# Kernel tuning notes

Hardware: AMD Instinct MI355X
Metric: run time of the kernel (lower is better)

Reference implementation:

```python
import jax, jax.numpy as jnp
from jax import lax
import numpy as np

NOTES = 78
IN_DIM = 80
T_HID = 64
N_HID = 2
B = 64
T = 128


def lstm_seq(x, w_ih, w_hh, b_ih, b_hh):
    """Batch-first single-layer LSTM from zero state.
    x: (N, S, D); w_ih: (4H, D); w_hh: (4H, H). Gate order i,f,g,o (PyTorch).
    Returns hidden outputs (N, S, H)."""
    H = w_hh.shape[1]
    N = x.shape[0]
    # precompute input contribution for all steps: (N, S, 4H)
    gx = jnp.einsum('nsd,gd->nsg', x, w_ih) + b_ih + b_hh

    def step(carry, g_t):
        h, c = carry
        g = g_t + h @ w_hh.T
        i, f, gg, o = jnp.split(g, 4, axis=-1)
        c = jax.nn.sigmoid(f) * c + jax.nn.sigmoid(i) * jnp.tanh(gg)
        h = jax.nn.sigmoid(o) * jnp.tanh(c)
        return (h, c), h

    h0 = jnp.zeros((N, H), x.dtype)
    (_, _), hs = lax.scan(step, (h0, h0), jnp.swapaxes(gx, 0, 1))
    return jnp.swapaxes(hs, 0, 1)  # (N, S, H)


def setup_inputs() -> dict:
    key = jax.random.key(0)
    ks = jax.random.split(key, 9)
    s = 1.0 / np.sqrt(T_HID)
    sn = 1.0 / np.sqrt(N_HID)
    u = lambda k, shp, sc: jax.random.uniform(k, shp, jnp.float32, -sc, sc)
    return {
        'x': jax.random.normal(ks[0], (B, NOTES, T, IN_DIM), jnp.float32),
        'w_ih_t': u(ks[1], (4 * T_HID, IN_DIM), s),
        'w_hh_t': u(ks[2], (4 * T_HID, T_HID), s),
        'b_ih_t': u(ks[3], (4 * T_HID,), s),
        'b_hh_t': u(ks[4], (4 * T_HID,), s),
        'w_ih_n': u(ks[5], (4 * N_HID, T_HID), sn),
        'w_hh_n': u(ks[6], (4 * N_HID, N_HID), sn),
        'b_ih_n': u(ks[7], (4 * N_HID,), sn),
        'b_hh_n': u(ks[8], (4 * N_HID,), sn),
    }


def reference(x, w_ih_t, w_hh_t, b_ih_t, b_hh_t, w_ih_n, w_hh_n, b_ih_n, b_hh_n):
    b, n_notes, t_len, _ = x.shape
    # Time LSTM: independent over (batch, note); sequence axis = time.
    xt = x.reshape(b * n_notes, t_len, IN_DIM)
    time_out = lstm_seq(xt, w_ih_t, w_hh_t, b_ih_t, b_hh_t)  # (B*78, T, H)
    time_out = time_out.reshape(b, n_notes, t_len, T_HID)
    # Note LSTM: run over the 78-note axis, fresh zero state at EVERY time step
    # (faithful to the original, which reuses self.hidden_note0 each iteration).
    xn = jnp.transpose(time_out, (0, 2, 1, 3)).reshape(b * t_len, n_notes, T_HID)
    note_out = lstm_seq(xn, w_ih_n, w_hh_n, b_ih_n, b_hh_n)  # (B*T, 78, 2)
    note_out = note_out.reshape(b, t_len, n_notes * N_HID)  # (B, T, 156)
    # Hard threshold, exactly as torch.where(x > 0.5, ones, zeros)
    return jnp.where(note_out > 0.5, jnp.ones_like(note_out), jnp.zeros_like(note_out))
```

## Files before the change

### kernel.cpp

```cpp
#include <hip/hip_runtime.h>
#include <math.h>

#define NOTES 78
#define IN_DIM 80
#define T_HID 64
#define N_HID 2
#define BATCH 64
#define TLEN 128
#define NSEQ (BATCH * NOTES)
#define NBT  (BATCH * TLEN)
#define SB   4

__device__ __forceinline__ float sigf(float x) { return 1.0f / (1.0f + expf(-x)); }
__device__ __forceinline__ float rdl(float v, int k) {
    return __int_as_float(__builtin_amdgcn_readlane(__float_as_int(v), k));
}

__global__ __launch_bounds__(256, 2)
void time_lstm_fused(const float* __restrict__ x,
                     const float* __restrict__ w_ih,
                     const float* __restrict__ w_hh,
                     const float* __restrict__ b_ih,
                     const float* __restrict__ b_hh,
                     const float* __restrict__ w_ih_n,
                     const float* __restrict__ b_ih_n,
                     const float* __restrict__ b_hh_n,
                     float* __restrict__ gxn) {
    __shared__ float hbuf[SB][T_HID];
    __shared__ float G0[SB][256];
    __shared__ float G1[SB][256];

    const int tid  = threadIdx.x;
    const int s0   = blockIdx.x * SB;
    const int wid  = tid >> 6;
    const int lane = tid & 63;
    const bool isx = (wid < 2);
    const int g0   = ((wid & 1) << 7) | (2 * lane);

    float4 wA[20], wB[20];
    float biasA = 0.0f, biasB = 0.0f;
    if (isx) {
        const float4* pA = (const float4*)(w_ih + (size_t)g0 * IN_DIM);
        const float4* pB = (const float4*)(w_ih + (size_t)(g0 + 1) * IN_DIM);
#pragma unroll
        for (int j = 0; j < 20; j++) { wA[j] = pA[j]; wB[j] = pB[j]; }
        biasA = b_ih[g0] + b_hh[g0];
        biasB = b_ih[g0 + 1] + b_hh[g0 + 1];
    } else {
        const float4* pA = (const float4*)(w_hh + (size_t)g0 * T_HID);
        const float4* pB = (const float4*)(w_hh + (size_t)(g0 + 1) * T_HID);
#pragma unroll
        for (int j = 0; j < 16; j++) { wA[j] = pA[j]; wB[j] = pB[j]; }
    }

    const float* xr[SB];
#pragma unroll
    for (int s = 0; s < SB; s++) xr[s] = x + (size_t)(s0 + s) * TLEN * IN_DIM;

    float xa[SB], xb[SB];
    if (isx) {
#pragma unroll
        for (int s = 0; s < SB; s++) {
            xa[s] = xr[s][lane];
            xb[s] = xr[s][64 + (lane & 15)];
        }
    }

    float cst = 0.0f;

    const int su2 = tid >> 6;
    const int nj  = (tid >> 3) & 7;
    const int nk  = tid & 7;
    float wn[8];
#pragma unroll
    for (int i = 0; i < 8; i++) wn[i] = w_ih_n[nj * 64 + nk * 8 + i];
    const float nbias = b_ih_n[nj] + b_hh_n[nj];
    const int sglb = s0 + su2;
    const int nb = sglb / NOTES, nn = sglb % NOTES;
    float* gout = gxn + ((size_t)nn * NBT + (size_t)nb * TLEN) * 8 + nj;

    hbuf[wid][lane] = 0.0f;
    __syncthreads();

    for (int t = 0; t < TLEN; t++) {
        if (t > 0) {
            float p = 0.0f;
#pragma unroll
            for (int i = 0; i < 8; i++) p = fmaf(wn[i], hbuf[su2][nk * 8 + i], p);
            p += __shfl_xor(p, 1);
            p += __shfl_xor(p, 2);
            p += __shfl_xor(p, 4);
            if (nk == 0) gout[(size_t)(t - 1) * 8] = p + nbias;
        }

        float xna[SB], xnb[SB];
        const bool pf = isx && (t + 1 < TLEN);
        if (pf) {
#pragma unroll
            for (int s = 0; s < SB; s++) {
                xna[s] = xr[s][(t + 1) * IN_DIM + lane];
                xnb[s] = xr[s][(t + 1) * IN_DIM + 64 + (lane & 15)];
            }
        }

        if (isx) {
            float aA[SB], aB[SB];
#pragma unroll
            for (int s = 0; s < SB; s++) { aA[s] = biasA; aB[s] = biasB; }
#pragma unroll
            for (int k4 = 0; k4 < 16; k4++) {
                const float4 vA = wA[k4], vB = wB[k4];
#pragma unroll
                for (int s = 0; s < SB; s++) {
                    const float r0 = rdl(xa[s], 4 * k4 + 0);
                    const float r1 = rdl(xa[s], 4 * k4 + 1);
                    const float r2 = rdl(xa[s], 4 * k4 + 2);
                    const float r3 = rdl(xa[s], 4 * k4 + 3);
                    aA[s] = fmaf(vA.x, r0, aA[s]);  aB[s] = fmaf(vB.x, r0, aB[s]);
                    aA[s] = fmaf(vA.y, r1, aA[s]);  aB[s] = fmaf(vB.y, r1, aB[s]);
                    aA[s] = fmaf(vA.z, r2, aA[s]);  aB[s] = fmaf(vB.z, r2, aB[s]);
                    aA[s] = fmaf(vA.w, r3, aA[s]);  aB[s] = fmaf(vB.w, r3, aB[s]);
                }
            }
#pragma unroll
            for (int k4 = 16; k4 < 20; k4++) {
                const float4 vA = wA[k4], vB = wB[k4];
#pragma unroll
                for (int s = 0; s < SB; s++) {
                    const float r0 = rdl(xb[s], 4 * k4 - 64);
                    const float r1 = rdl(xb[s], 4 * k4 - 63);
                    const float r2 = rdl(xb[s], 4 * k4 - 62);
                    const float r3 = rdl(xb[s], 4 * k4 - 61);
                    aA[s] = fmaf(vA.x, r0, aA[s]);  aB[s] = fmaf(vB.x, r0, aB[s]);
                    aA[s] = fmaf(vA.y, r1, aA[s]);  aB[s] = fmaf(vB.y, r1, aB[s]);
                    aA[s] = fmaf(vA.z, r2, aA[s]);  aB[s] = fmaf(vB.z, r2, aB[s]);
                    aA[s] = fmaf(vA.w, r3, aA[s]);  aB[s] = fmaf(vB.w, r3, aB[s]);
                }
            }
#pragma unroll
            for (int s = 0; s < SB; s++) {
                *(float2*)&G0[s][g0] = make_float2(aA[s], aB[s]);
            }
        } else {
            float hv[SB];
#pragma unroll
            for (int s = 0; s < SB; s++) hv[s] = hbuf[s][lane];
            float aA[SB], aB[SB];
#pragma unroll
            for (int s = 0; s < SB; s++) { aA[s] = 0.0f; aB[s] = 0.0f; }
#pragma unroll
            for (int k4 = 0; k4 < 16; k4++) {
                const float4 vA = wA[k4], vB = wB[k4];
#pragma unroll
                for (int s = 0; s < SB; s++) {
                    const float r0 = rdl(hv[s], 4 * k4 + 0);
                    const float r1 = rdl(hv[s], 4 * k4 + 1);
                    const float r2 = rdl(hv[s], 4 * k4 + 2);
                    const float r3 = rdl(hv[s], 4 * k4 + 3);
                    aA[s] = fmaf(vA.x, r0, aA[s]);  aB[s] = fmaf(vB.x, r0, aB[s]);
                    aA[s] = fmaf(vA.y, r1, aA[s]);  aB[s] = fmaf(vB.y, r1, aB[s]);
                    aA[s] = fmaf(vA.z, r2, aA[s]);  aB[s] = fmaf(vB.z, r2, aB[s]);
                    aA[s] = fmaf(vA.w, r3, aA[s]);  aB[s] = fmaf(vB.w, r3, aB[s]);
                }
            }
#pragma unroll
            for (int s = 0; s < SB; s++) {
                *(float2*)&G1[s][g0] = make_float2(aA[s], aB[s]);
            }
        }
        __syncthreads();

        {
            const float i_p = G0[wid][lane]       + G1[wid][lane];
            const float f_p = G0[wid][64 + lane]  + G1[wid][64 + lane];
            const float g_p = G0[wid][128 + lane] + G1[wid][128 + lane];
            const float o_p = G0[wid][192 + lane] + G1[wid][192 + lane];
            cst = sigf(f_p) * cst + sigf(i_p) * tanhf(g_p);
            const float h = sigf(o_p) * tanhf(cst);
            hbuf[wid][lane] = h;
        }
        if (pf) {
#pragma unroll
            for (int s = 0; s < SB; s++) { xa[s] = xna[s]; xb[s] = xnb[s]; }
        }
        __syncthreads();
    }

    {
        float p = 0.0f;
#pragma unroll
        for (int i = 0; i < 8; i++) p = fmaf(wn[i], hbuf[su2][nk * 8 + i], p);
        p += __shfl_xor(p, 1);
        p += __shfl_xor(p, 2);
        p += __shfl_xor(p, 4);
        if (nk == 0) gout[(size_t)(TLEN - 1) * 8] = p + nbias;
    }
}

__global__ __launch_bounds__(64)
void note_scan_kernel(const float* __restrict__ gxn,
                      const float* __restrict__ w_hh_n,
                      float* __restrict__ out) {
    const int bt = blockIdx.x * 64 + threadIdx.x;
    float wh[16];
#pragma unroll
    for (int i = 0; i < 16; i++) wh[i] = w_hh_n[i];
    float h0 = 0.f, h1 = 0.f, c0 = 0.f, c1 = 0.f;

    const float4* gp = (const float4*)gxn;
    float res[2 * NOTES];

    size_t idx = (size_t)bt * 2;
    float4 ga = gp[idx], gb = gp[idx + 1];
    for (int n = 0; n < NOTES; n++) {
        float4 na, nb2;
        if (n + 1 < NOTES) {
            const size_t nidx = ((size_t)(n + 1) * NBT + bt) * 2;
            na  = gp[nidx];
            nb2 = gp[nidx + 1];
        }
        const float i0 = ga.x + wh[0]  * h0 + wh[1]  * h1;
        const float i1 = ga.y + wh[2]  * h0 + wh[3]  * h1;
        const float f0 = ga.z + wh[4]  * h0 + wh[5]  * h1;
        const float f1 = ga.w + wh[6]  * h0 + wh[7]  * h1;
        const float g0 = gb.x + wh[8]  * h0 + wh[9]  * h1;
        const float g1 = gb.y + wh[10] * h0 + wh[11] * h1;
        const float o0 = gb.z + wh[12] * h0 + wh[13] * h1;
        const float o1 = gb.w + wh[14] * h0 + wh[15] * h1;
        c0 = sigf(f0) * c0 + sigf(i0) * tanhf(g0);
        c1 = sigf(f1) * c1 + sigf(i1) * tanhf(g1);
        h0 = sigf(o0) * tanhf(c0);
        h1 = sigf(o1) * tanhf(c1);
        res[n * 2 + 0] = (h0 > 0.5f) ? 1.0f : 0.0f;
        res[n * 2 + 1] = (h1 > 0.5f) ? 1.0f : 0.0f;
        ga = na; gb = nb2;
    }
    float4* op = (float4*)(out + (size_t)bt * (NOTES * N_HID));
#pragma unroll
    for (int j = 0; j < (2 * NOTES) / 4; j++) {
        op[j] = make_float4(res[4 * j], res[4 * j + 1], res[4 * j + 2], res[4 * j + 3]);
    }
}

extern "C" void kernel_launch(void* const* d_in, const int* in_sizes, int n_in,
                              void* d_out, int out_size, void* d_ws, size_t ws_size,
                              hipStream_t stream) {
    const float* x      = (const float*)d_in[0];
    const float* w_ih_t = (const float*)d_in[1];
    const float* w_hh_t = (const float*)d_in[2];
    const float* b_ih_t = (const float*)d_in[3];
    const float* b_hh_t = (const float*)d_in[4];
    const float* w_ih_n = (const float*)d_in[5];
    const float* w_hh_n = (const float*)d_in[6];
    const float* b_ih_n = (const float*)d_in[7];
    const float* b_hh_n = (const float*)d_in[8];
    float* out = (float*)d_out;

    float* gxn = (float*)d_ws;

    time_lstm_fused<<<NSEQ / SB, 256, 0, stream>>>(
        x, w_ih_t, w_hh_t, b_ih_t, b_hh_t, w_ih_n, b_ih_n, b_hh_n, gxn);
    note_scan_kernel<<<NBT / 64, 64, 0, stream>>>(gxn, w_hh_n, out);
}
```

Measured before the change: 1.354 ms.

## Split LSTM gate dot products across K-halves with 512-thread blocks

Doubles the time-LSTM block to 8 waves, so each wave handles half of the reduction dimension for the input and recurrent matvecs. Partial sums go to separate shared buffers and are added by the recurrent waves before the gate nonlinearity. This halves per-wave weight registers and serial FMA/readlane chains per step, which shortens the sequential critical path and may raise occupancy. The cost is extra shared-memory traffic and larger blocks. The note-scan kernel is also changed to write results incrementally as float4 instead of buffering 156 values in a register array.

```diff
diff --git a/kernel.cpp b/kernel.cpp
--- a/kernel.cpp
+++ b/kernel.cpp
@@ -16,7 +16,7 @@
     return __int_as_float(__builtin_amdgcn_readlane(__float_as_int(v), k));
 }
 
-__global__ __launch_bounds__(256, 2)
+__global__ __launch_bounds__(512, 4)
 void time_lstm_fused(const float* __restrict__ x,
                      const float* __restrict__ w_ih,
                      const float* __restrict__ w_hh,
@@ -27,88 +27,79 @@
                      const float* __restrict__ b_hh_n,
                      float* __restrict__ gxn) {
     __shared__ float hbuf[SB][T_HID];
-    __shared__ float G0[SB][256];
-    __shared__ float G1[SB][256];
+    __shared__ float Gx[2][SB][256];
+    __shared__ float Gh[2][SB][256];
 
     const int tid  = threadIdx.x;
     const int s0   = blockIdx.x * SB;
     const int wid  = tid >> 6;
     const int lane = tid & 63;
-    const bool isx = (wid < 2);
-    const int g0   = ((wid & 1) << 7) | (2 * lane);
-
-    float4 wA[20], wB[20];
+    const bool isx = (wid < 4);
+    const int lw   = isx ? wid : (wid - 4);
+    const int kh   = lw >> 1;
+    const int gh   = lw & 1;
+    const int g0   = (gh << 7) | (2 * lane);
+
+    float4 wA[10], wB[10];
     float biasA = 0.0f, biasB = 0.0f;
     if (isx) {
-        const float4* pA = (const float4*)(w_ih + (size_t)g0 * IN_DIM);
-        const float4* pB = (const float4*)(w_ih + (size_t)(g0 + 1) * IN_DIM);
-#pragma unroll
-        for (int j = 0; j < 20; j++) { wA[j] = pA[j]; wB[j] = pB[j]; }
-        biasA = b_ih[g0] + b_hh[g0];
-        biasB = b_ih[g0 + 1] + b_hh[g0 + 1];
+        const float4* pA = (const float4*)(w_ih + (size_t)g0 * IN_DIM + 40 * kh);
+        const float4* pB = (const float4*)(w_ih + (size_t)(g0 + 1) * IN_DIM + 40 * kh);
+#pragma unroll
+        for (int j = 0; j < 10; j++) { wA[j] = pA[j]; wB[j] = pB[j]; }
+        if (kh == 0) {
+            biasA = b_ih[g0] + b_hh[g0];
+            biasB = b_ih[g0 + 1] + b_hh[g0 + 1];
+        }
     } else {
-        const float4* pA = (const float4*)(w_hh + (size_t)g0 * T_HID);
-        const float4* pB = (const float4*)(w_hh + (size_t)(g0 + 1) * T_HID);
-#pragma unroll
-        for (int j = 0; j < 16; j++) { wA[j] = pA[j]; wB[j] = pB[j]; }
+        const float4* pA = (const float4*)(w_hh + (size_t)g0 * T_HID + 32 * kh);
+        const float4* pB = (const float4*)(w_hh + (size_t)(g0 + 1) * T_HID + 32 * kh);
+#pragma unroll
+        for (int j = 0; j < 8; j++) { wA[j] = pA[j]; wB[j] = pB[j]; }
     }
 
     const float* xr[SB];
 #pragma unroll
     for (int s = 0; s < SB; s++) xr[s] = x + (size_t)(s0 + s) * TLEN * IN_DIM;
 
-    float xa[SB], xb[SB];
+    const int ol = 40 * kh + (lane < 39 ? lane : 39);
+
+    float xa[SB], xna[SB];
     if (isx) {
 #pragma unroll
-        for (int s = 0; s < SB; s++) {
-            xa[s] = xr[s][lane];
-            xb[s] = xr[s][64 + (lane & 15)];
-        }
+        for (int s = 0; s < SB; s++) xa[s] = xr[s][ol];
     }
 
     float cst = 0.0f;
-
-    const int su2 = tid >> 6;
-    const int nj  = (tid >> 3) & 7;
-    const int nk  = tid & 7;
+    const int hol = (kh << 5) | (lane & 31);
+    const int nj = (lane >> 3) & 7;
+    const int nk = lane & 7;
     float wn[8];
-#pragma unroll
-    for (int i = 0; i < 8; i++) wn[i] = w_ih_n[nj * 64 + nk * 8 + i];
-    const float nbias = b_ih_n[nj] + b_hh_n[nj];
-    const int sglb = s0 + su2;
-    const int nb = sglb / NOTES, nn = sglb % NOTES;
-    float* gout = gxn + ((size_t)nn * NBT + (size_t)nb * TLEN) * 8 + nj;
-
-    hbuf[wid][lane] = 0.0f;
+    float nbias = 0.0f;
+    float* gout = gxn;
+    if (!isx) {
+#pragma unroll
+        for (int i = 0; i < 8; i++) wn[i] = w_ih_n[nj * 64 + nk * 8 + i];
+        nbias = b_ih_n[nj] + b_hh_n[nj];
+        const int sglb = s0 + lw;
+        const int nb = sglb / NOTES, nn = sglb % NOTES;
+        gout = gxn + ((size_t)nn * NBT + (size_t)nb * TLEN) * 8 + nj;
+    }
+
+    if (tid < SB * T_HID) hbuf[tid >> 6][tid & 63] = 0.0f;
     __syncthreads();
 
     for (int t = 0; t < TLEN; t++) {
-        if (t > 0) {
-            float p = 0.0f;
-#pragma unroll
-            for (int i = 0; i < 8; i++) p = fmaf(wn[i], hbuf[su2][nk * 8 + i], p);
-            p += __shfl_xor(p, 1);
-            p += __shfl_xor(p, 2);
-            p += __shfl_xor(p, 4);
-            if (nk == 0) gout[(size_t)(t - 1) * 8] = p + nbias;
-        }
-
-        float xna[SB], xnb[SB];
-        const bool pf = isx && (t + 1 < TLEN);
-        if (pf) {
-#pragma unroll
-            for (int s = 0; s < SB; s++) {
-                xna[s] = xr[s][(t + 1) * IN_DIM + lane];
-                xnb[s] = xr[s][(t + 1) * IN_DIM + 64 + (lane & 15)];
-            }
-        }
-
         if (isx) {
+            if (t + 1 < TLEN) {
+#pragma unroll
+                for (int s = 0; s < SB; s++) xna[s] = xr[s][(t + 1) * IN_DIM + ol];
+            }
             float aA[SB], aB[SB];
 #pragma unroll
             for (int s = 0; s < SB; s++) { aA[s] = biasA; aB[s] = biasB; }
 #pragma unroll
-            for (int k4 = 0; k4 < 16; k4++) {
+            for (int k4 = 0; k4 < 10; k4++) {
                 const float4 vA = wA[k4], vB = wB[k4];
 #pragma unroll
                 for (int s = 0; s < SB; s++) {
@@ -123,33 +114,26 @@
                 }
             }
 #pragma unroll
-            for (int k4 = 16; k4 < 20; k4++) {
-                const float4 vA = wA[k4], vB = wB[k4];
-#pragma unroll
-                for (int s = 0; s < SB; s++) {
-                    const float r0 = rdl(xb[s], 4 * k4 - 64);
-                    const float r1 = rdl(xb[s], 4 * k4 - 63);
-                    const float r2 = rdl(xb[s], 4 * k4 - 62);
-                    const float r3 = rdl(xb[s], 4 * k4 - 61);
-                    aA[s] = fmaf(vA.x, r0, aA[s]);  aB[s] = fmaf(vB.x, r0, aB[s]);
-                    aA[s] = fmaf(vA.y, r1, aA[s]);  aB[s] = fmaf(vB.y, r1, aB[s]);
-                    aA[s] = fmaf(vA.z, r2, aA[s]);  aB[s] = fmaf(vB.z, r2, aB[s]);
-                    aA[s] = fmaf(vA.w, r3, aA[s]);  aB[s] = fmaf(vB.w, r3, aB[s]);
-                }
-            }
-#pragma unroll
-            for (int s = 0; s < SB; s++) {
-                *(float2*)&G0[s][g0] = make_float2(aA[s], aB[s]);
-            }
+            for (int s = 0; s < SB; s++)
+                *(float2*)&Gx[kh][s][g0] = make_float2(aA[s], aB[s]);
         } else {
+            if (t > 0) {
+                float p = 0.0f;
+#pragma unroll
+                for (int i = 0; i < 8; i++) p = fmaf(wn[i], hbuf[lw][nk * 8 + i], p);
+                p += __shfl_xor(p, 1);
+                p += __shfl_xor(p, 2);
+                p += __shfl_xor(p, 4);
+                if (nk == 0) gout[(size_t)(t - 1) * 8] = p + nbias;
+            }
             float hv[SB];
 #pragma unroll
-            for (int s = 0; s < SB; s++) hv[s] = hbuf[s][lane];
+            for (int s = 0; s < SB; s++) hv[s] = hbuf[s][hol];
             float aA[SB], aB[SB];
 #pragma unroll
             for (int s = 0; s < SB; s++) { aA[s] = 0.0f; aB[s] = 0.0f; }
 #pragma unroll
-            for (int k4 = 0; k4 < 16; k4++) {
+            for (int k4 = 0; k4 < 8; k4++) {
                 const float4 vA = wA[k4], vB = wB[k4];
 #pragma unroll
                 for (int s = 0; s < SB; s++) {
@@ -164,32 +148,34 @@
                 }
             }
 #pragma unroll
-            for (int s = 0; s < SB; s++) {
-                *(float2*)&G1[s][g0] = make_float2(aA[s], aB[s]);
-            }
+            for (int s = 0; s < SB; s++)
+                *(float2*)&Gh[kh][s][g0] = make_float2(aA[s], aB[s]);
         }
         __syncthreads();
 
-        {
-            const float i_p = G0[wid][lane]       + G1[wid][lane];
-            const float f_p = G0[wid][64 + lane]  + G1[wid][64 + lane];
-            const float g_p = G0[wid][128 + lane] + G1[wid][128 + lane];
-            const float o_p = G0[wid][192 + lane] + G1[wid][192 + lane];
+        if (!isx) {
+            const float i_p = Gx[0][lw][lane]       + Gx[1][lw][lane]
+                            + Gh[0][lw][lane]       + Gh[1][lw][lane];
+            const float f_p = Gx[0][lw][64 + lane]  + Gx[1][lw][64 + lane]
+                            + Gh[0][lw][64 + lane]  + Gh[1][lw][64 + lane];
+            const float g_p = Gx[0][lw][128 + lane] + Gx[1][lw][128 + lane]
+                            + Gh[0][lw][128 + lane] + Gh[1][lw][128 + lane];
+            const float o_p = Gx[0][lw][192 + lane] + Gx[1][lw][192 + lane]
+                            + Gh[0][lw][192 + lane] + Gh[1][lw][192 + lane];
             cst = sigf(f_p) * cst + sigf(i_p) * tanhf(g_p);
             const float h = sigf(o_p) * tanhf(cst);
-            hbuf[wid][lane] = h;
-        }
-        if (pf) {
-#pragma unroll
-            for (int s = 0; s < SB; s++) { xa[s] = xna[s]; xb[s] = xnb[s]; }
+            hbuf[lw][lane] = h;
+        } else if (t + 1 < TLEN) {
+#pragma unroll
+            for (int s = 0; s < SB; s++) xa[s] = xna[s];
         }
         __syncthreads();
     }
 
-    {
+    if (!isx) {
         float p = 0.0f;
 #pragma unroll
-        for (int i = 0; i < 8; i++) p = fmaf(wn[i], hbuf[su2][nk * 8 + i], p);
+        for (int i = 0; i < 8; i++) p = fmaf(wn[i], hbuf[lw][nk * 8 + i], p);
         p += __shfl_xor(p, 1);
         p += __shfl_xor(p, 2);
         p += __shfl_xor(p, 4);
@@ -208,37 +194,38 @@
     float h0 = 0.f, h1 = 0.f, c0 = 0.f, c1 = 0.f;
 
     const float4* gp = (const float4*)gxn;
-    float res[2 * NOTES];
+    float4* op = (float4*)(out + (size_t)bt * (NOTES * N_HID));
 
     size_t idx = (size_t)bt * 2;
     float4 ga = gp[idx], gb = gp[idx + 1];
-    for (int n = 0; n < NOTES; n++) {
-        float4 na, nb2;
-        if (n + 1 < NOTES) {
-            const size_t nidx = ((size_t)(n + 1) * NBT + bt) * 2;
-            na  = gp[nidx];
-            nb2 = gp[nidx + 1];
-        }
-        const float i0 = ga.x + wh[0]  * h0 + wh[1]  * h1;
-        const float i1 = ga.y + wh[2]  * h0 + wh[3]  * h1;
-        const float f0 = ga.z + wh[4]  * h0 + wh[5]  * h1;
-        const float f1 = ga.w + wh[6]  * h0 + wh[7]  * h1;
-        const float g0 = gb.x + wh[8]  * h0 + wh[9]  * h1;
-        const float g1 = gb.y + wh[10] * h0 + wh[11] * h1;
-        const float o0 = gb.z + wh[12] * h0 + wh[13] * h1;
-        const float o1 = gb.w + wh[14] * h0 + wh[15] * h1;
-        c0 = sigf(f0) * c0 + sigf(i0) * tanhf(g0);
-        c1 = sigf(f1) * c1 + sigf(i1) * tanhf(g1);
-        h0 = sigf(o0) * tanhf(c0);
-        h1 = sigf(o1) * tanhf(c1);
-        res[n * 2 + 0] = (h0 > 0.5f) ? 1.0f : 0.0f;
-        res[n * 2 + 1] = (h1 > 0.5f) ? 1.0f : 0.0f;
-        ga = na; gb = nb2;
-    }
-    float4* op = (float4*)(out + (size_t)bt * (NOTES * N_HID));
-#pragma unroll
-    for (int j = 0; j < (2 * NOTES) / 4; j++) {
-        op[j] = make_float4(res[4 * j], res[4 * j + 1], res[4 * j + 2], res[4 * j + 3]);
+    for (int n0 = 0; n0 < NOTES; n0 += 2) {
+        float r[4];
+#pragma unroll
+        for (int u = 0; u < 2; u++) {
+            const int n = n0 + u;
+            float4 na, nb2;
+            if (n + 1 < NOTES) {
+                const size_t nidx = ((size_t)(n + 1) * NBT + bt) * 2;
+                na  = gp[nidx];
+                nb2 = gp[nidx + 1];
+            }
+            const float i0 = ga.x + wh[0]  * h0 + wh[1]  * h1;
+            const float i1 = ga.y + wh[2]  * h0 + wh[3]  * h1;
+            const float f0 = ga.z + wh[4]  * h0 + wh[5]  * h1;
+            const float f1 = ga.w + wh[6]  * h0 + wh[7]  * h1;
+            const float g0 = gb.x + wh[8]  * h0 + wh[9]  * h1;
+            const float g1 = gb.y + wh[10] * h0 + wh[11] * h1;
+            const float o0 = gb.z + wh[12] * h0 + wh[13] * h1;
+            const float o1 = gb.w + wh[14] * h0 + wh[15] * h1;
+            c0 = sigf(f0) * c0 + sigf(i0) * tanhf(g0);
+            c1 = sigf(f1) * c1 + sigf(i1) * tanhf(g1);
+            h0 = sigf(o0) * tanhf(c0);
+            h1 = sigf(o1) * tanhf(c1);
+            r[2 * u + 0] = (h0 > 0.5f) ? 1.0f : 0.0f;
+            r[2 * u + 1] = (h1 > 0.5f) ? 1.0f : 0.0f;
+            ga = na; gb = nb2;
+        }
+        op[n0 >> 1] = make_float4(r[0], r[1], r[2], r[3]);
     }
 }
 
@@ -258,7 +245,7 @@
 
     float* gxn = (float*)d_ws;
 
-    time_lstm_fused<<<NSEQ / SB, 256, 0, stream>>>(
+    time_lstm_fused<<<NSEQ / SB, 512, 0, stream>>>(
         x, w_ih_t, w_hh_t, b_ih_t, b_hh_t, w_ih_n, b_ih_n, b_hh_n, gxn);
     note_scan_kernel<<<NBT / 64, 64, 0, stream>>>(gxn, w_hh_n, out);
 }
```

Result: faster. 1.310 ms (-3.3%).
